# Kernel optimization log

Hardware: AMD Instinct MI355X
Metric: run time of the kernel (lower is better)

## Reference

```python
import jax, jax.numpy as jnp
import numpy as np

DIM = 256
HEADS = 8
HEAD_DIM = DIM // HEADS
SCALE = HEAD_DIM ** -0.5
EPS_LN = 1e-5
EPS_NORM = 1e-12


def setup_inputs() -> dict:
    key = jax.random.key(0)
    ks = jax.random.split(key, 12)
    B, C, H, W = 8, DIM, 32, 32
    s = 0.02
    return {
        "x": jax.random.normal(ks[0], (B, C, H, W), jnp.float32),
        "dw_w": jax.random.normal(ks[1], (C, 1, 3, 3), jnp.float32) * s,
        "dw_b": jnp.zeros((C,), jnp.float32),
        "qkv_w": jax.random.normal(ks[2], (3 * C, C), jnp.float32) * s,
        "c1_w": jax.random.normal(ks[3], (C, C), jnp.float32) * s,
        "c1_b": jnp.zeros((C,), jnp.float32),
        "ln1_g": jnp.ones((C,), jnp.float32),
        "ln1_b": jnp.zeros((C,), jnp.float32),
        "c2_w": jax.random.normal(ks[4], (C, C), jnp.float32) * s,
        "c2_b": jnp.zeros((C,), jnp.float32),
        "ln2_g": jnp.ones((C,), jnp.float32),
        "ln2_b": jnp.zeros((C,), jnp.float32),
    }


def _l2norm(t):
    n = jnp.sqrt(jnp.sum(t * t, axis=-1, keepdims=True))
    return t / jnp.maximum(n, EPS_NORM)


def _layernorm_c(x_nchw, g, b):
    # LayerNorm over channel dim of an NCHW tensor (torch does permute->LN->permute)
    mu = jnp.mean(x_nchw, axis=1, keepdims=True)
    var = jnp.mean((x_nchw - mu) ** 2, axis=1, keepdims=True)
    xn = (x_nchw - mu) * jax.lax.rsqrt(var + EPS_LN)
    return xn * g[None, :, None, None] + b[None, :, None, None]


def _gelu(x):
    return jax.nn.gelu(x, approximate=False)


def reference(x, dw_w, dw_b, qkv_w, c1_w, c1_b, ln1_g, ln1_b, c2_w, c2_b, ln2_g, ln2_b):
    B, C, H, W = x.shape
    identity = x
    # depthwise 3x3 conv
    y = jax.lax.conv_general_dilated(
        x, dw_w, window_strides=(1, 1), padding="SAME",
        dimension_numbers=("NCHW", "OIHW", "NCHW"), feature_group_count=C)
    y = y + dw_b[None, :, None, None]
    # tokens [B, N, C]
    t = y.reshape(B, C, H * W).transpose(0, 2, 1)
    qkv = jnp.einsum("bnc,oc->bno", t, qkv_w)  # [B,N,3C]
    qkv = qkv.reshape(B, H * W, 3, HEADS, HEAD_DIM).transpose(2, 0, 3, 1, 4)
    q, k, v = qkv[0], qkv[1], qkv[2]  # [B,h,N,d]
    q = _l2norm(q)
    k = _l2norm(k)
    attn = jnp.einsum("bhnd,bhmd->bhnm", q, k) * SCALE
    attn = jax.nn.softmax(attn, axis=-1)
    o = jnp.einsum("bhnm,bhmd->bhnd", attn, v)  # [B,h,N,d]
    o = o.transpose(0, 2, 1, 3).reshape(B, H * W, C)
    y = o.transpose(0, 2, 1).reshape(B, C, H, W)
    # conv-MLP branch (1x1 convs as channel GEMMs)
    y = jnp.einsum("bchw,oc->bohw", y, c1_w) + c1_b[None, :, None, None]
    y = _gelu(_layernorm_c(y, ln1_g, ln1_b))
    y = jnp.einsum("bchw,oc->bohw", y, c2_w) + c2_b[None, :, None, None]
    y = _gelu(_layernorm_c(y, ln2_g, ln2_b))
    return identity + y
```

## Files before the change

### kernel.cpp

```cpp
#include <hip/hip_runtime.h>
#include <math.h>

#define DIMC 256
#define NTOK 1024
#define QKVN 768
#define HDIM 32

typedef __attribute__((ext_vector_type(8))) short bf16x8;
typedef __attribute__((ext_vector_type(4))) float f32x4;
typedef __attribute__((ext_vector_type(4))) unsigned short us4;

__device__ __forceinline__ unsigned short f2bf(float f) {
  unsigned u = __float_as_uint(f);
  u += 0x7FFF + ((u >> 16) & 1);
  return (unsigned short)(u >> 16);
}

__device__ __forceinline__ float gelu_f(float y) {
  return 0.5f * y * (1.f + erff(y * 0.70710678118654752f));
}

__global__ __launch_bounds__(256) void dwt_k(const float* __restrict__ x,
                                             const float* __restrict__ w,
                                             const float* __restrict__ b,
                                             unsigned short* __restrict__ A0,
                                             const float* __restrict__ w0,
                                             const float* __restrict__ w1,
                                             const float* __restrict__ w2,
                                             unsigned short* __restrict__ Wb) {
  int blk = blockIdx.x;
  int t = threadIdx.x;
  if (blk >= 2048) {
    int i = ((blk - 2048) * 256 + t) * 4;
    const float* src;
    int off;
    if (i < 196608) { src = w0; off = i; }
    else if (i < 262144) { src = w1; off = i - 196608; }
    else { src = w2; off = i - 262144; }
    float4 v = *(const float4*)(src + off);
    us4 o = {f2bf(v.x), f2bf(v.y), f2bf(v.z), f2bf(v.w)};
    *(us4*)(Wb + i) = o;
    return;
  }
  __shared__ float xs[32][3][33];
  __shared__ float ws9[32][9];
  __shared__ float bs[32];
  const int b_ = blk >> 8, h = (blk >> 3) & 31, c0 = (blk & 7) << 5;
  {
    int cl = t >> 3, seg = (t & 7) << 2;
    const float* xp = x + ((size_t)(b_ * 256 + c0 + cl) << 10);
#pragma unroll
    for (int dh = 0; dh < 3; dh++) {
      int h2 = h + dh - 1;
      float4 v = {0.f, 0.f, 0.f, 0.f};
      if ((unsigned)h2 < 32u) v = *(const float4*)(xp + h2 * 32 + seg);
      xs[cl][dh][seg + 0] = v.x; xs[cl][dh][seg + 1] = v.y;
      xs[cl][dh][seg + 2] = v.z; xs[cl][dh][seg + 3] = v.w;
    }
  }
  for (int i = t; i < 288; i += 256) ws9[i / 9][i % 9] = w[(c0 + i / 9) * 9 + i % 9];
  if (t < 32) bs[t] = b[c0 + t];
  __syncthreads();
  const int wp = t >> 3, cq = (t & 7) << 2;
  us4 o;
#pragma unroll
  for (int j = 0; j < 4; j++) {
    int c = cq + j;
    float acc = bs[c];
#pragma unroll
    for (int dh = 0; dh < 3; dh++) {
#pragma unroll
      for (int dw = 0; dw < 3; dw++) {
        int w2 = wp + dw - 1;
        if ((unsigned)w2 < 32u) acc += xs[c][dh][w2] * ws9[c][dh * 3 + dw];
      }
    }
    o[j] = f2bf(acc);
  }
  *(us4*)(A0 + (((size_t)(b_ * 1024 + h * 32 + wp)) << 8) + c0 + cq) = o;
}

template <bool BIAS>
__global__ __launch_bounds__(256) void mgemm_k(const unsigned short* __restrict__ A,
                                               const unsigned short* __restrict__ W,
                                               const float* __restrict__ bias,
                                               float* __restrict__ C, int N) {
  __shared__ __align__(16) unsigned short As[128 * 40];
  __shared__ __align__(16) unsigned short Bs[64 * 40];
  const int t = threadIdx.x;
  const int m0 = blockIdx.y * 128;
  const int n0 = blockIdx.x * 64;
  const int wid = t >> 6, lane = t & 63;
  const int lg = lane >> 4, lr = lane & 15;
  const int wm0 = (wid >> 1) * 64, wn0 = (wid & 1) * 32;

  f32x4 acc[4][2] = {};
  for (int k0 = 0; k0 < 256; k0 += 32) {
    __syncthreads();
    {
#pragma unroll
      for (int u = 0; u < 2; u++) {
        int f = t + u * 256;
        int r = f >> 2, c = f & 3;
        bf16x8 v = *(const bf16x8*)(A + (size_t)(m0 + r) * 256 + k0 + c * 8);
        *(bf16x8*)&As[r * 40 + c * 8] = v;
      }
      int o = t >> 2, c = t & 3;
      bf16x8 v = *(const bf16x8*)(W + (size_t)(n0 + o) * 256 + k0 + c * 8);
      *(bf16x8*)&Bs[o * 40 + c * 8] = v;
    }
    __syncthreads();
    bf16x8 af[4], bfr[2];
#pragma unroll
    for (int mt = 0; mt < 4; mt++)
      af[mt] = *(const bf16x8*)&As[(wm0 + mt * 16 + lr) * 40 + lg * 8];
#pragma unroll
    for (int nt = 0; nt < 2; nt++)
      bfr[nt] = *(const bf16x8*)&Bs[(wn0 + nt * 16 + lr) * 40 + lg * 8];
#pragma unroll
    for (int mt = 0; mt < 4; mt++)
#pragma unroll
      for (int nt = 0; nt < 2; nt++)
        acc[mt][nt] = __builtin_amdgcn_mfma_f32_16x16x32_bf16(af[mt], bfr[nt], acc[mt][nt], 0, 0, 0);
  }
  float bv[2];
#pragma unroll
  for (int nt = 0; nt < 2; nt++)
    bv[nt] = BIAS ? bias[n0 + wn0 + nt * 16 + lr] : 0.f;
#pragma unroll
  for (int mt = 0; mt < 4; mt++)
#pragma unroll
    for (int nt = 0; nt < 2; nt++)
#pragma unroll
      for (int r = 0; r < 4; r++) {
        int row = m0 + wm0 + mt * 16 + lg * 4 + r;
        int col = n0 + wn0 + nt * 16 + lr;
        C[(size_t)row * N + col] = acc[mt][nt][r] + bv[nt];
      }
}

#define VPAD 66
__global__ __launch_bounds__(256) void qkvprep_k(const float* __restrict__ qkv,
                                                 unsigned short* __restrict__ Qb,
                                                 unsigned short* __restrict__ Kb,
                                                 unsigned short* __restrict__ Vt) {
  __shared__ unsigned short Vl[32 * VPAD];
  const int tt = blockIdx.x, bh = blockIdx.y;
  const int b = bh >> 3, h = bh & 7;
  const int n0 = tt * 64;
  const int t = threadIdx.x;
  {
    int pair = t >> 7, idx = t & 127;
    int nl = idx >> 1, e0 = (idx & 1) << 4;
    const float* p = qkv + (size_t)(b * 1024 + n0 + nl) * QKVN + pair * 256 + h * 32 + e0;
    float4 v0 = *(const float4*)(p + 0);
    float4 v1 = *(const float4*)(p + 4);
    float4 v2 = *(const float4*)(p + 8);
    float4 v3 = *(const float4*)(p + 12);
    float s = v0.x * v0.x + v0.y * v0.y + v0.z * v0.z + v0.w * v0.w
            + v1.x * v1.x + v1.y * v1.y + v1.z * v1.z + v1.w * v1.w
            + v2.x * v2.x + v2.y * v2.y + v2.z * v2.z + v2.w * v2.w
            + v3.x * v3.x + v3.y * v3.y + v3.z * v3.z + v3.w * v3.w;
    s += __shfl_xor(s, 1, 64);
    float inv = 1.f / fmaxf(sqrtf(s), 1e-12f);
    if (pair == 0) inv *= 0.17677669529663687f;
    unsigned short* dst = (pair ? Kb : Qb) + ((size_t)(bh * 1024 + n0 + nl)) * 32 + e0;
    us4 o0 = {f2bf(v0.x * inv), f2bf(v0.y * inv), f2bf(v0.z * inv), f2bf(v0.w * inv)};
    us4 o1 = {f2bf(v1.x * inv), f2bf(v1.y * inv), f2bf(v1.z * inv), f2bf(v1.w * inv)};
    us4 o2 = {f2bf(v2.x * inv), f2bf(v2.y * inv), f2bf(v2.z * inv), f2bf(v2.w * inv)};
    us4 o3 = {f2bf(v3.x * inv), f2bf(v3.y * inv), f2bf(v3.z * inv), f2bf(v3.w * inv)};
    *(us4*)(dst + 0) = o0; *(us4*)(dst + 4) = o1;
    *(us4*)(dst + 8) = o2; *(us4*)(dst + 12) = o3;
  }
  {
    int nl = t >> 2, d8 = (t & 3) * 8;
    const float* p = qkv + (size_t)(b * 1024 + n0 + nl) * QKVN + 512 + h * 32 + d8;
    float4 a = *(const float4*)p;
    float4 c = *(const float4*)(p + 4);
    float vv[8] = {a.x, a.y, a.z, a.w, c.x, c.y, c.z, c.w};
#pragma unroll
    for (int i = 0; i < 8; i++) Vl[(d8 + i) * VPAD + nl] = f2bf(vv[i]);
  }
  __syncthreads();
  {
    int d = t >> 3, seg = t & 7;
    us4 lo = *(const us4*)&Vl[d * VPAD + seg * 8];
    us4 hi = *(const us4*)&Vl[d * VPAD + seg * 8 + 4];
    unsigned short* dst = Vt + ((size_t)(bh * 32 + d) << 10) + n0 + seg * 8;
    *(us4*)dst = lo;
    *(us4*)(dst + 4) = hi;
  }
}

#define PSTR 36

__global__ __launch_bounds__(64) void attn_mfma_k(const unsigned short* __restrict__ Qb,
                                                  const unsigned short* __restrict__ Kb,
                                                  const unsigned short* __restrict__ Vt,
                                                  unsigned short* __restrict__ obuf) {
  __shared__ __align__(16) unsigned short Pl[32 * PSTR];
  const int bh = blockIdx.y;
  const int q0 = blockIdx.x * 32;
  const int lane = threadIdx.x;
  const int lg = lane >> 4, lr = lane & 15;
  const size_t base = (size_t)bh * NTOK;
  const unsigned short* vb = Vt + ((size_t)bh * 32 << 10);

  bf16x8 qf[2];
#pragma unroll
  for (int qt = 0; qt < 2; qt++)
    qf[qt] = *(const bf16x8*)(Qb + (base + q0 + qt * 16 + lr) * 32 + lg * 8);

  f32x4 o[2][2] = {};
  float lpart[2][4] = {};

  for (int step = 0; step < 32; step++) {
    const int kv0 = step * 32;
    bf16x8 kf[2];
#pragma unroll
    for (int ct = 0; ct < 2; ct++)
      kf[ct] = *(const bf16x8*)(Kb + (base + kv0 + ct * 16 + lr) * 32 + lg * 8);
#pragma unroll
    for (int qt = 0; qt < 2; qt++) {
#pragma unroll
      for (int ct = 0; ct < 2; ct++) {
        f32x4 c = {};
        c = __builtin_amdgcn_mfma_f32_16x16x32_bf16(qf[qt], kf[ct], c, 0, 0, 0);
#pragma unroll
        for (int r = 0; r < 4; r++) {
          float p = __expf(c[r]);
          lpart[qt][r] += p;
          Pl[(qt * 16 + lg * 4 + r) * PSTR + ct * 16 + lr] = f2bf(p);
        }
      }
    }
#pragma unroll
    for (int qt = 0; qt < 2; qt++) {
      us4 plo = *(const us4*)&Pl[(qt * 16 + lr) * PSTR + lg * 8];
      us4 phi = *(const us4*)&Pl[(qt * 16 + lr) * PSTR + lg * 8 + 4];
      bf16x8 pf = {(short)plo[0], (short)plo[1], (short)plo[2], (short)plo[3],
                   (short)phi[0], (short)phi[1], (short)phi[2], (short)phi[3]};
#pragma unroll
      for (int dt = 0; dt < 2; dt++) {
        bf16x8 vf = *(const bf16x8*)(vb + ((size_t)(dt * 16 + lr) << 10) + kv0 + lg * 8);
        o[qt][dt] = __builtin_amdgcn_mfma_f32_16x16x32_bf16(pf, vf, o[qt][dt], 0, 0, 0);
      }
    }
  }
#pragma unroll
  for (int qt = 0; qt < 2; qt++) {
#pragma unroll
    for (int r = 0; r < 4; r++) {
      float l = lpart[qt][r];
      l += __shfl_xor(l, 1, 64); l += __shfl_xor(l, 2, 64);
      l += __shfl_xor(l, 4, 64); l += __shfl_xor(l, 8, 64);
      lpart[qt][r] = 1.f / l;
    }
  }
  const int b = bh >> 3, h = bh & 7;
#pragma unroll
  for (int qt = 0; qt < 2; qt++)
#pragma unroll
    for (int dt = 0; dt < 2; dt++)
#pragma unroll
      for (int r = 0; r < 4; r++) {
        int q = q0 + qt * 16 + lg * 4 + r;
        int c = h * 32 + dt * 16 + lr;
        obuf[((size_t)(b * NTOK + q)) * DIMC + c] = f2bf(o[qt][dt][r] * lpart[qt][r]);
      }
}

__global__ void ln_gelu_k(const float* __restrict__ in, const float* __restrict__ g,
                          const float* __restrict__ bb, unsigned short* __restrict__ out) {
  int t = threadIdx.x;
  int lane = t & 63;
  int r = blockIdx.x * 4 + (t >> 6);
  const float* p = in + ((size_t)r << 8) + (lane << 2);
  float4 v = *(const float4*)p;
  float s1 = v.x + v.y + v.z + v.w;
  float s2 = v.x * v.x + v.y * v.y + v.z * v.z + v.w * v.w;
#pragma unroll
  for (int m = 1; m < 64; m <<= 1) {
    s1 += __shfl_xor(s1, m, 64);
    s2 += __shfl_xor(s2, m, 64);
  }
  float mu = s1 * (1.f / 256.f);
  float var = s2 * (1.f / 256.f) - mu * mu;
  float rstd = rsqrtf(var + 1e-5f);
  float4 gv = *(const float4*)(g + (lane << 2));
  float4 bv = *(const float4*)(bb + (lane << 2));
  us4 ob = {f2bf(gelu_f((v.x - mu) * rstd * gv.x + bv.x)),
            f2bf(gelu_f((v.y - mu) * rstd * gv.y + bv.y)),
            f2bf(gelu_f((v.z - mu) * rstd * gv.z + bv.z)),
            f2bf(gelu_f((v.w - mu) * rstd * gv.w + bv.w))};
  *(us4*)(out + ((size_t)r << 8) + (lane << 2)) = ob;
}

__global__ __launch_bounds__(256) void ln_trans_k(const float* __restrict__ in,
                                                  const float* __restrict__ g,
                                                  const float* __restrict__ bb,
                                                  const float* __restrict__ x,
                                                  float* __restrict__ out) {
  __shared__ float ys[32][257];
  const int b = blockIdx.y, s0 = blockIdx.x << 5;
  const int t = threadIdx.x, lane = t & 63, wv = t >> 6;
  float gv[4], bv[4];
#pragma unroll
  for (int e = 0; e < 4; e++) { gv[e] = g[lane + 64 * e]; bv[e] = bb[lane + 64 * e]; }
  for (int i = 0; i < 8; i++) {
    int tok = wv * 8 + i;
    size_t r = (size_t)(b * 1024 + s0 + tok) << 8;
    float v[4];
    float s1 = 0.f, s2 = 0.f;
#pragma unroll
    for (int e = 0; e < 4; e++) {
      v[e] = in[r + lane + 64 * e];
      s1 += v[e]; s2 += v[e] * v[e];
    }
#pragma unroll
    for (int m = 1; m < 64; m <<= 1) {
      s1 += __shfl_xor(s1, m, 64);
      s2 += __shfl_xor(s2, m, 64);
    }
    float mu = s1 * (1.f / 256.f);
    float var = s2 * (1.f / 256.f) - mu * mu;
    float rstd = rsqrtf(var + 1e-5f);
#pragma unroll
    for (int e = 0; e < 4; e++)
      ys[tok][lane + 64 * e] = gelu_f((v[e] - mu) * rstd * gv[e] + bv[e]);
  }
  __syncthreads();
  const int j = t & 31, cr = t >> 5;
  for (int c = cr; c < 256; c += 8) {
    size_t idx = ((size_t)(b * 256 + c) << 10) + s0 + j;
    out[idx] = x[idx] + ys[j][c];
  }
}

extern "C" void kernel_launch(void* const* d_in, const int* in_sizes, int n_in,
                              void* d_out, int out_size, void* d_ws, size_t ws_size,
                              hipStream_t stream) {
  const float* x     = (const float*)d_in[0];
  const float* dw_w  = (const float*)d_in[1];
  const float* dw_b  = (const float*)d_in[2];
  const float* qkv_w = (const float*)d_in[3];
  const float* c1_w  = (const float*)d_in[4];
  const float* c1_b  = (const float*)d_in[5];
  const float* ln1_g = (const float*)d_in[6];
  const float* ln1_b = (const float*)d_in[7];
  const float* c2_w  = (const float*)d_in[8];
  const float* c2_b  = (const float*)d_in[9];
  const float* ln2_g = (const float*)d_in[10];
  const float* ln2_b = (const float*)d_in[11];
  float* out = (float*)d_out;

  float* ws = (float*)d_ws;
  const size_t MF = (size_t)1 << 20;
  unsigned short* Wb = (unsigned short*)ws;
  unsigned short* A0 = (unsigned short*)(ws + MF / 4);
  float* qkv  = ws + 2 * MF;
  unsigned short* Qb = (unsigned short*)(ws + 8 * MF);
  unsigned short* Kb = (unsigned short*)(ws + 9 * MF);
  unsigned short* Vtb = (unsigned short*)(ws + 10 * MF);
  unsigned short* obuf = (unsigned short*)(ws + MF / 4);
  float* buf1 = ws + 2 * MF;
  unsigned short* m1 = (unsigned short*)(ws + 4 * MF);
  float* buf2 = ws + 5 * MF;
  (void)in_sizes; (void)n_in; (void)out_size; (void)ws_size;

  dwt_k<<<2368, 256, 0, stream>>>(x, dw_w, dw_b, A0, qkv_w, c1_w, c2_w, Wb);
  mgemm_k<false><<<dim3(12, 64), 256, 0, stream>>>(A0, Wb, nullptr, qkv, 768);
  qkvprep_k<<<dim3(16, 64), 256, 0, stream>>>(qkv, Qb, Kb, Vtb);
  attn_mfma_k<<<dim3(32, 64), 64, 0, stream>>>(Qb, Kb, Vtb, obuf);
  mgemm_k<true><<<dim3(4, 64), 256, 0, stream>>>(obuf, Wb + 196608, c1_b, buf1, 256);
  ln_gelu_k<<<2048, 256, 0, stream>>>(buf1, ln1_g, ln1_b, m1);
  mgemm_k<true><<<dim3(4, 64), 256, 0, stream>>>(m1, Wb + 262144, c2_b, buf2, 256);
  ln_trans_k<<<dim3(32, 8), 256, 0, stream>>>(buf2, ln2_g, ln2_b, x, out);
}
```

Before: 169.5 us.

## Fuse QKV prep (L2 norm, scale, V transpose) into QKV GEMM epilogue

Replaces the QKV GEMM plus separate qkvprep kernel with one GEMM whose epilogue L2-normalizes Q/K per head via lane shuffles, applies the softmax scale, and writes bf16 Q, K and transposed V directly. This removes the fp32 qkv intermediate round-trip through memory and one launch. Epilogue stores are scalar 2-byte writes for Q/K, which may coalesce less well. The workspace layout is reshuffled to match.

```diff
diff --git a/kernel.cpp b/kernel.cpp
--- a/kernel.cpp
+++ b/kernel.cpp
@@ -80,6 +80,87 @@
   *(us4*)(A0 + (((size_t)(b_ * 1024 + h * 32 + wp)) << 8) + c0 + cq) = o;
 }
 
+__global__ __launch_bounds__(256) void mgemm_qkv_k(const unsigned short* __restrict__ A,
+                                                   const unsigned short* __restrict__ W,
+                                                   unsigned short* __restrict__ Qb,
+                                                   unsigned short* __restrict__ Kb,
+                                                   unsigned short* __restrict__ Vt) {
+  __shared__ __align__(16) unsigned short As[128 * 40];
+  __shared__ __align__(16) unsigned short Bs[64 * 40];
+  const int t = threadIdx.x;
+  const int m0 = blockIdx.x * 128;
+  const int n0 = blockIdx.y * 64;
+  const int wid = t >> 6, lane = t & 63;
+  const int lg = lane >> 4, lr = lane & 15;
+  const int wm0 = (wid >> 1) * 64, wn0 = (wid & 1) * 32;
+
+  f32x4 acc[4][2] = {};
+  for (int k0 = 0; k0 < 256; k0 += 32) {
+    __syncthreads();
+    {
+#pragma unroll
+      for (int u = 0; u < 2; u++) {
+        int f = t + u * 256;
+        int r = f >> 2, c = f & 3;
+        bf16x8 v = *(const bf16x8*)(A + (size_t)(m0 + r) * 256 + k0 + c * 8);
+        *(bf16x8*)&As[r * 40 + c * 8] = v;
+      }
+      int o = t >> 2, c = t & 3;
+      bf16x8 v = *(const bf16x8*)(W + (size_t)(n0 + o) * 256 + k0 + c * 8);
+      *(bf16x8*)&Bs[o * 40 + c * 8] = v;
+    }
+    __syncthreads();
+    bf16x8 af[4], bfr[2];
+#pragma unroll
+    for (int mt = 0; mt < 4; mt++)
+      af[mt] = *(const bf16x8*)&As[(wm0 + mt * 16 + lr) * 40 + lg * 8];
+#pragma unroll
+    for (int nt = 0; nt < 2; nt++)
+      bfr[nt] = *(const bf16x8*)&Bs[(wn0 + nt * 16 + lr) * 40 + lg * 8];
+#pragma unroll
+    for (int mt = 0; mt < 4; mt++)
+#pragma unroll
+      for (int nt = 0; nt < 2; nt++)
+        acc[mt][nt] = __builtin_amdgcn_mfma_f32_16x16x32_bf16(af[mt], bfr[nt], acc[mt][nt], 0, 0, 0);
+  }
+  const int b_ = m0 >> 10;
+  const int nr0 = (m0 & 1023) + wm0;
+  const int sec = n0 >> 8;
+  const int h = ((n0 & 255) + wn0) >> 5;
+  const int bh = b_ * 8 + h;
+  if (sec < 2) {
+    unsigned short* dst = (sec == 0 ? Qb : Kb);
+    const float scl = (sec == 0) ? 0.17677669529663687f : 1.f;
+#pragma unroll
+    for (int mt = 0; mt < 4; mt++) {
+#pragma unroll
+      for (int r = 0; r < 4; r++) {
+        float s = acc[mt][0][r] * acc[mt][0][r] + acc[mt][1][r] * acc[mt][1][r];
+        s += __shfl_xor(s, 1, 64); s += __shfl_xor(s, 2, 64);
+        s += __shfl_xor(s, 4, 64); s += __shfl_xor(s, 8, 64);
+        float inv = scl / fmaxf(sqrtf(s), 1e-12f);
+        int tok = nr0 + mt * 16 + lg * 4 + r;
+        size_t rowoff = ((size_t)(bh << 10) + tok) * 32;
+#pragma unroll
+        for (int nt = 0; nt < 2; nt++)
+          dst[rowoff + nt * 16 + lr] = f2bf(acc[mt][nt][r] * inv);
+      }
+    }
+  } else {
+#pragma unroll
+    for (int mt = 0; mt < 4; mt++) {
+      int tok0 = nr0 + mt * 16 + lg * 4;
+#pragma unroll
+      for (int nt = 0; nt < 2; nt++) {
+        int d = nt * 16 + lr;
+        us4 o = {f2bf(acc[mt][nt][0]), f2bf(acc[mt][nt][1]),
+                 f2bf(acc[mt][nt][2]), f2bf(acc[mt][nt][3])};
+        *(us4*)(Vt + (((size_t)(bh * 32 + d)) << 10) + tok0) = o;
+      }
+    }
+  }
+}
+
 template <bool BIAS>
 __global__ __launch_bounds__(256) void mgemm_k(const unsigned short* __restrict__ A,
                                                const unsigned short* __restrict__ W,
@@ -137,59 +218,6 @@
         int col = n0 + wn0 + nt * 16 + lr;
         C[(size_t)row * N + col] = acc[mt][nt][r] + bv[nt];
       }
-}
-
-#define VPAD 66
-__global__ __launch_bounds__(256) void qkvprep_k(const float* __restrict__ qkv,
-                                                 unsigned short* __restrict__ Qb,
-                                                 unsigned short* __restrict__ Kb,
-                                                 unsigned short* __restrict__ Vt) {
-  __shared__ unsigned short Vl[32 * VPAD];
-  const int tt = blockIdx.x, bh = blockIdx.y;
-  const int b = bh >> 3, h = bh & 7;
-  const int n0 = tt * 64;
-  const int t = threadIdx.x;
-  {
-    int pair = t >> 7, idx = t & 127;
-    int nl = idx >> 1, e0 = (idx & 1) << 4;
-    const float* p = qkv + (size_t)(b * 1024 + n0 + nl) * QKVN + pair * 256 + h * 32 + e0;
-    float4 v0 = *(const float4*)(p + 0);
-    float4 v1 = *(const float4*)(p + 4);
-    float4 v2 = *(const float4*)(p + 8);
-    float4 v3 = *(const float4*)(p + 12);
-    float s = v0.x * v0.x + v0.y * v0.y + v0.z * v0.z + v0.w * v0.w
-            + v1.x * v1.x + v1.y * v1.y + v1.z * v1.z + v1.w * v1.w
-            + v2.x * v2.x + v2.y * v2.y + v2.z * v2.z + v2.w * v2.w
-            + v3.x * v3.x + v3.y * v3.y + v3.z * v3.z + v3.w * v3.w;
-    s += __shfl_xor(s, 1, 64);
-    float inv = 1.f / fmaxf(sqrtf(s), 1e-12f);
-    if (pair == 0) inv *= 0.17677669529663687f;
-    unsigned short* dst = (pair ? Kb : Qb) + ((size_t)(bh * 1024 + n0 + nl)) * 32 + e0;
-    us4 o0 = {f2bf(v0.x * inv), f2bf(v0.y * inv), f2bf(v0.z * inv), f2bf(v0.w * inv)};
-    us4 o1 = {f2bf(v1.x * inv), f2bf(v1.y * inv), f2bf(v1.z * inv), f2bf(v1.w * inv)};
-    us4 o2 = {f2bf(v2.x * inv), f2bf(v2.y * inv), f2bf(v2.z * inv), f2bf(v2.w * inv)};
-    us4 o3 = {f2bf(v3.x * inv), f2bf(v3.y * inv), f2bf(v3.z * inv), f2bf(v3.w * inv)};
-    *(us4*)(dst + 0) = o0; *(us4*)(dst + 4) = o1;
-    *(us4*)(dst + 8) = o2; *(us4*)(dst + 12) = o3;
-  }
-  {
-    int nl = t >> 2, d8 = (t & 3) * 8;
-    const float* p = qkv + (size_t)(b * 1024 + n0 + nl) * QKVN + 512 + h * 32 + d8;
-    float4 a = *(const float4*)p;
-    float4 c = *(const float4*)(p + 4);
-    float vv[8] = {a.x, a.y, a.z, a.w, c.x, c.y, c.z, c.w};
-#pragma unroll
-    for (int i = 0; i < 8; i++) Vl[(d8 + i) * VPAD + nl] = f2bf(vv[i]);
-  }
-  __syncthreads();
-  {
-    int d = t >> 3, seg = t & 7;
-    us4 lo = *(const us4*)&Vl[d * VPAD + seg * 8];
-    us4 hi = *(const us4*)&Vl[d * VPAD + seg * 8 + 4];
-    unsigned short* dst = Vt + ((size_t)(bh * 32 + d) << 10) + n0 + seg * 8;
-    *(us4*)dst = lo;
-    *(us4*)(dst + 4) = hi;
-  }
 }
 
 #define PSTR 36
@@ -358,19 +386,17 @@
   const size_t MF = (size_t)1 << 20;
   unsigned short* Wb = (unsigned short*)ws;
   unsigned short* A0 = (unsigned short*)(ws + MF / 4);
-  float* qkv  = ws + 2 * MF;
-  unsigned short* Qb = (unsigned short*)(ws + 8 * MF);
-  unsigned short* Kb = (unsigned short*)(ws + 9 * MF);
-  unsigned short* Vtb = (unsigned short*)(ws + 10 * MF);
+  unsigned short* Qb = (unsigned short*)(ws + 2 * MF);
+  unsigned short* Kb = (unsigned short*)(ws + 3 * MF);
+  unsigned short* Vtb = (unsigned short*)(ws + 4 * MF);
   unsigned short* obuf = (unsigned short*)(ws + MF / 4);
-  float* buf1 = ws + 2 * MF;
-  unsigned short* m1 = (unsigned short*)(ws + 4 * MF);
-  float* buf2 = ws + 5 * MF;
+  float* buf1 = ws + 5 * MF;
+  unsigned short* m1 = (unsigned short*)(ws + 7 * MF);
+  float* buf2 = ws + 8 * MF;
   (void)in_sizes; (void)n_in; (void)out_size; (void)ws_size;
 
   dwt_k<<<2368, 256, 0, stream>>>(x, dw_w, dw_b, A0, qkv_w, c1_w, c2_w, Wb);
-  mgemm_k<false><<<dim3(12, 64), 256, 0, stream>>>(A0, Wb, nullptr, qkv, 768);
-  qkvprep_k<<<dim3(16, 64), 256, 0, stream>>>(qkv, Qb, Kb, Vtb);
+  mgemm_qkv_k<<<dim3(64, 12), 256, 0, stream>>>(A0, Wb, Qb, Kb, Vtb);
   attn_mfma_k<<<dim3(32, 64), 64, 0, stream>>>(Qb, Kb, Vtb, obuf);
   mgemm_k<true><<<dim3(4, 64), 256, 0, stream>>>(obuf, Wb + 196608, c1_b, buf1, 256);
   ln_gelu_k<<<2048, 256, 0, stream>>>(buf1, ln1_g, ln1_b, m1);
```

New measurement: 161.5 us. -4.8%, faster.
